# Performance work log

Measured on AMD Instinct MI355X. Metric: run time of the kernel, lower is better.

## Reference

```python
import jax, jax.numpy as jnp
import numpy as np

HIDDEN = 512
WINDOW = 5  # window_size default
NEG = -1000000000.0  # masked_fill value in the original


def setup_inputs() -> dict:
    key = jax.random.key(0)
    k0, k1, k2, k3, k4 = jax.random.split(key, 5)
    B, S, H = 32, 4096, HIDDEN
    decoder_hidden = jax.random.normal(k0, (B, H), dtype=jnp.float32)
    encoder_outputs = jax.random.normal(k1, (B, S, H), dtype=jnp.float32)
    input_lengths = jax.random.randint(k2, (B,), 1, S + 1)
    # position_network: nn.Linear(H, 1) -> weight [1,H], bias [1]
    Wp = jax.random.normal(k3, (1, H), dtype=jnp.float32) * (1.0 / np.sqrt(H))
    bp = jnp.zeros((1,), dtype=jnp.float32)
    # W_a: nn.Linear(H, H, bias=False) -> weight [H,H]
    Wa = jax.random.normal(k4, (H, H), dtype=jnp.float32) * (1.0 / np.sqrt(H))
    return {
        "decoder_hidden": decoder_hidden,
        "encoder_outputs": encoder_outputs,
        "Wp": Wp,
        "bp": bp,
        "Wa": Wa,
        "input_lengths": input_lengths,
    }


def reference(decoder_hidden, encoder_outputs, Wp, bp, Wa, input_lengths):
    B, S, H = encoder_outputs.shape
    half = WINDOW // 2

    # predicted window center: sigmoid(Linear(dh)) * S, truncated to int
    pos = jax.nn.sigmoid(decoder_hidden @ Wp.T + bp)[:, 0] * S  # [B]
    center = jnp.floor(pos).astype(jnp.int32)                   # int(...) on >=0 floats
    left = jnp.maximum(0, center - half)                        # [B]
    right = jnp.minimum(S, center + half + 1)                   # [B]

    idx = jnp.arange(S)                                         # [S]
    window_mask = (idx[None, :] >= left[:, None]) & (idx[None, :] < right[:, None])

    # 'general' score: dh_i @ (W_a enc_j) == (dh_i @ Wa) . enc_j
    q = decoder_hidden @ Wa                                     # [B,H]
    scores = jnp.einsum('bh,bsh->bs', q, encoder_outputs)       # [B,S]
    scores = jnp.where(window_mask, scores, 0.0)                # zeros outside window

    valid = idx[None, :] < input_lengths[:, None]               # length mask
    scores = jnp.where(valid, scores, NEG)

    attention_weights = jax.nn.softmax(scores, axis=1)          # [B,S]
    context_vector = jnp.einsum('bs,bsh->bh', attention_weights, encoder_outputs)
    return context_vector, attention_weights
```

## Files before the change

kernel.cpp:

```cpp
#include <hip/hip_runtime.h>

#define BB 32
#define SS 4096
#define HH 512
#define HALF 2


__global__ __launch_bounds__(256) void prep_kernel(
    const float* __restrict__ dh, const float* __restrict__ enc,
    const float* __restrict__ Wp, const float* __restrict__ bp,
    const float* __restrict__ Wa, const int* __restrict__ lens,
    float* __restrict__ wpar, int* __restrict__ ipar)
{
    int b = blockIdx.x;
    int tid = threadIdx.x;
    __shared__ float s_dh[HH];
    __shared__ float s_q[HH];
    __shared__ float red[256];
    __shared__ float s_scores[8];
    __shared__ int s_left, s_right, s_rend;

    for (int i = tid; i < HH; i += 256) s_dh[i] = dh[b * HH + i];
    __syncthreads();

    float p = 0.f;
    for (int i = tid; i < HH; i += 256) p += s_dh[i] * Wp[i];
    red[tid] = p;
    __syncthreads();
    for (int o = 128; o > 0; o >>= 1) {
        if (tid < o) red[tid] += red[tid + o];
        __syncthreads();
    }
    if (tid == 0) {
        float x = red[0] + bp[0];
        float sig = 1.f / (1.f + expf(-x));
        float pos = sig * (float)SS;
        int center = (int)floorf(pos);
        int left = center - HALF; if (left < 0) left = 0;
        int right = center + HALF + 1; if (right > SS) right = SS;
        int len = lens[b];
        s_left = left;
        s_right = right;
        s_rend = (right < len) ? right : len;
    }
    __syncthreads();

    for (int j = tid; j < HH; j += 256) {
        float acc = 0.f;
        #pragma unroll 8
        for (int i = 0; i < HH; ++i) acc += s_dh[i] * Wa[i * HH + j];
        s_q[j] = acc;
    }
    __syncthreads();

    int wave = tid >> 6, lane = tid & 63;
    const float* encb = enc + (size_t)b * SS * HH;
    for (int wi = wave; wi < 5; wi += 4) {
        int s = s_left + wi;
        float sc = 0.f;
        if (s < s_right) {
            const float* row = encb + (size_t)s * HH;
            for (int i = lane; i < HH; i += 64) sc += s_q[i] * row[i];
        }
        #pragma unroll
        for (int o = 32; o > 0; o >>= 1) sc += __shfl_down(sc, o);
        if (lane == 0) s_scores[wi] = sc;
    }
    __syncthreads();

    if (tid == 0) {
        int len = lens[b];
        int nwin = s_rend - s_left; if (nwin < 0) nwin = 0;
        int nonwin = len - nwin;
        float m = (nonwin > 0) ? 0.f : -3.0e38f;
        for (int i = 0; i < nwin; ++i) m = fmaxf(m, s_scores[i]);
        float e0 = expf(-m);
        float Z = (float)nonwin * e0;
        float wv[5];
        #pragma unroll
        for (int i = 0; i < 5; ++i) wv[i] = 0.f;
        for (int i = 0; i < nwin; ++i) { wv[i] = expf(s_scores[i] - m); Z += wv[i]; }
        float inv = 1.f / Z;
        wpar[b * 8 + 0] = e0 * inv;
        #pragma unroll
        for (int i = 0; i < 5; ++i) wpar[b * 8 + 1 + i] = wv[i] * inv;
        ipar[b * 4 + 0] = s_left;
        ipar[b * 4 + 1] = s_rend;
        ipar[b * 4 + 2] = len;
    }
}

__global__ __launch_bounds__(256) void weights_kernel(
    const float* __restrict__ wpar, const int* __restrict__ ipar,
    float* __restrict__ wout)
{
    int idx = blockIdx.x * 256 + threadIdx.x;
    int b = idx >> 12;
    int s = idx & (SS - 1);
    int left = ipar[b * 4 + 0];
    int rend = ipar[b * 4 + 1];
    int len  = ipar[b * 4 + 2];
    float w;
    if (s >= len) w = 0.f;
    else if (s >= left && s < rend) w = wpar[b * 8 + 1 + (s - left)];
    else w = wpar[b * 8];
    wout[idx] = w;
}

#define CS 64

__global__ __launch_bounds__(256) void context_kernel(
    const float* __restrict__ enc, const float* __restrict__ wpar,
    const int* __restrict__ ipar, float* __restrict__ ctx)
{
    const int nchunks = SS / CS;
    int b = blockIdx.x / nchunks;
    int chunk = blockIdx.x % nchunks;
    int len = ipar[b * 4 + 2];
    int s0 = chunk * CS;
    if (s0 >= len) return;
    int s1 = s0 + CS; if (s1 > len) s1 = len;
    int left = ipar[b * 4 + 0];
    int rend = ipar[b * 4 + 1];
    float c = wpar[b * 8];

    int tid = threadIdx.x;
    int col = tid & 127;
    int rp = tid >> 7;
    const float4* enc4 = (const float4*)(enc + (size_t)b * SS * HH);

    float4 acc = make_float4(0.f, 0.f, 0.f, 0.f);
    for (int s = s0 + rp; s < s1; s += 2) {
        float w = c;
        if (s >= left && s < rend) w = wpar[b * 8 + 1 + (s - left)];
        float4 v = enc4[(size_t)s * (HH / 4) + col];
        acc.x += w * v.x; acc.y += w * v.y; acc.z += w * v.z; acc.w += w * v.w;
    }

    __shared__ float4 part[128];
    if (rp == 1) part[col] = acc;
    __syncthreads();
    if (rp == 0) {
        float4 o = part[col];
        acc.x += o.x; acc.y += o.y; acc.z += o.z; acc.w += o.w;
        float* dst = ctx + b * HH + col * 4;
        atomicAdd(dst + 0, acc.x);
        atomicAdd(dst + 1, acc.y);
        atomicAdd(dst + 2, acc.z);
        atomicAdd(dst + 3, acc.w);
    }
}

extern "C" void kernel_launch(void* const* d_in, const int* in_sizes, int n_in,
                              void* d_out, int out_size, void* d_ws, size_t ws_size,
                              hipStream_t stream)
{
    const float* dh   = (const float*)d_in[0];
    const float* enc  = (const float*)d_in[1];
    const float* Wp   = (const float*)d_in[2];
    const float* bp   = (const float*)d_in[3];
    const float* Wa   = (const float*)d_in[4];
    const int*   lens = (const int*)d_in[5];

    float* ctx  = (float*)d_out;
    float* wout = (float*)d_out + BB * HH;

    float* wpar = (float*)d_ws;
    int*   ipar = (int*)((char*)d_ws + BB * 8 * sizeof(float));

    hipMemsetAsync(d_out, 0, BB * HH * sizeof(float), stream);

    prep_kernel<<<BB, 256, 0, stream>>>(dh, enc, Wp, bp, Wa, lens, wpar, ipar);
    weights_kernel<<<BB * SS / 256, 256, 0, stream>>>(wpar, ipar, wout);
    context_kernel<<<BB * (SS / CS), 256, 0, stream>>>(enc, wpar, ipar, ctx);
}
```

Before: 412.4 us.

## Fuse weights and context kernels, fold ctx zeroing into prep, widen prep block

New measurement: 376.5 us. 8.7% less time.

```diff
diff --git a/kernel.cpp b/kernel.cpp
--- a/kernel.cpp
+++ b/kernel.cpp
@@ -4,30 +4,31 @@
 #define SS 4096
 #define HH 512
 #define HALF 2
+#define CS 64
 
 
-__global__ __launch_bounds__(256) void prep_kernel(
+__global__ __launch_bounds__(512) void prep_kernel(
     const float* __restrict__ dh, const float* __restrict__ enc,
     const float* __restrict__ Wp, const float* __restrict__ bp,
     const float* __restrict__ Wa, const int* __restrict__ lens,
-    float* __restrict__ wpar, int* __restrict__ ipar)
+    float* __restrict__ wpar, int* __restrict__ ipar, float* __restrict__ ctx)
 {
     int b = blockIdx.x;
     int tid = threadIdx.x;
     __shared__ float s_dh[HH];
     __shared__ float s_q[HH];
-    __shared__ float red[256];
+    __shared__ float red[512];
     __shared__ float s_scores[8];
-    __shared__ int s_left, s_right, s_rend;
+    __shared__ int s_left, s_rend;
 
-    for (int i = tid; i < HH; i += 256) s_dh[i] = dh[b * HH + i];
+    ctx[b * HH + tid] = 0.f;
+
+    s_dh[tid] = dh[b * HH + tid];
     __syncthreads();
 
-    float p = 0.f;
-    for (int i = tid; i < HH; i += 256) p += s_dh[i] * Wp[i];
-    red[tid] = p;
+    red[tid] = s_dh[tid] * Wp[tid];
     __syncthreads();
-    for (int o = 128; o > 0; o >>= 1) {
+    for (int o = 256; o > 0; o >>= 1) {
         if (tid < o) red[tid] += red[tid + o];
         __syncthreads();
     }
@@ -40,31 +41,29 @@
         int right = center + HALF + 1; if (right > SS) right = SS;
         int len = lens[b];
         s_left = left;
-        s_right = right;
         s_rend = (right < len) ? right : len;
     }
     __syncthreads();
 
-    for (int j = tid; j < HH; j += 256) {
+    {
         float acc = 0.f;
         #pragma unroll 8
-        for (int i = 0; i < HH; ++i) acc += s_dh[i] * Wa[i * HH + j];
-        s_q[j] = acc;
+        for (int i = 0; i < HH; ++i) acc += s_dh[i] * Wa[i * HH + tid];
+        s_q[tid] = acc;
     }
     __syncthreads();
 
     int wave = tid >> 6, lane = tid & 63;
-    const float* encb = enc + (size_t)b * SS * HH;
-    for (int wi = wave; wi < 5; wi += 4) {
-        int s = s_left + wi;
+    if (wave < 5) {
+        int s = s_left + wave;
         float sc = 0.f;
-        if (s < s_right) {
-            const float* row = encb + (size_t)s * HH;
+        if (s < s_rend) {
+            const float* row = enc + (size_t)b * SS * HH + (size_t)s * HH;
             for (int i = lane; i < HH; i += 64) sc += s_q[i] * row[i];
         }
         #pragma unroll
         for (int o = 32; o > 0; o >>= 1) sc += __shfl_down(sc, o);
-        if (lane == 0) s_scores[wi] = sc;
+        if (lane == 0) s_scores[wave] = sc;
     }
     __syncthreads();
 
@@ -90,41 +89,32 @@
     }
 }
 
-__global__ __launch_bounds__(256) void weights_kernel(
-    const float* __restrict__ wpar, const int* __restrict__ ipar,
+__global__ __launch_bounds__(256) void ctxw_kernel(
+    const float* __restrict__ enc, const float* __restrict__ wpar,
+    const int* __restrict__ ipar, float* __restrict__ ctx,
     float* __restrict__ wout)
 {
-    int idx = blockIdx.x * 256 + threadIdx.x;
-    int b = idx >> 12;
-    int s = idx & (SS - 1);
+    int b = blockIdx.x >> 6;
+    int chunk = blockIdx.x & 63;
+    int s0 = chunk * CS;
     int left = ipar[b * 4 + 0];
     int rend = ipar[b * 4 + 1];
     int len  = ipar[b * 4 + 2];
-    float w;
-    if (s >= len) w = 0.f;
-    else if (s >= left && s < rend) w = wpar[b * 8 + 1 + (s - left)];
-    else w = wpar[b * 8];
-    wout[idx] = w;
-}
+    float c = wpar[b * 8];
+    int tid = threadIdx.x;
 
-#define CS 64
+    if (tid < CS) {
+        int s = s0 + tid;
+        float w;
+        if (s >= len) w = 0.f;
+        else if (s >= left && s < rend) w = wpar[b * 8 + 1 + (s - left)];
+        else w = c;
+        wout[b * SS + s] = w;
+    }
 
-__global__ __launch_bounds__(256) void context_kernel(
-    const float* __restrict__ enc, const float* __restrict__ wpar,
-    const int* __restrict__ ipar, float* __restrict__ ctx)
-{
-    const int nchunks = SS / CS;
-    int b = blockIdx.x / nchunks;
-    int chunk = blockIdx.x % nchunks;
-    int len = ipar[b * 4 + 2];
-    int s0 = chunk * CS;
     if (s0 >= len) return;
     int s1 = s0 + CS; if (s1 > len) s1 = len;
-    int left = ipar[b * 4 + 0];
-    int rend = ipar[b * 4 + 1];
-    float c = wpar[b * 8];
 
-    int tid = threadIdx.x;
     int col = tid & 127;
     int rp = tid >> 7;
     const float4* enc4 = (const float4*)(enc + (size_t)b * SS * HH);
@@ -168,9 +158,6 @@
     float* wpar = (float*)d_ws;
     int*   ipar = (int*)((char*)d_ws + BB * 8 * sizeof(float));
 
-    hipMemsetAsync(d_out, 0, BB * HH * sizeof(float), stream);
-
-    prep_kernel<<<BB, 256, 0, stream>>>(dh, enc, Wp, bp, Wa, lens, wpar, ipar);
-    weights_kernel<<<BB * SS / 256, 256, 0, stream>>>(wpar, ipar, wout);
-    context_kernel<<<BB * (SS / CS), 256, 0, stream>>>(enc, wpar, ipar, ctx);
+    prep_kernel<<<BB, 512, 0, stream>>>(dh, enc, Wp, bp, Wa, lens, wpar, ipar, ctx);
+    ctxw_kernel<<<BB * (SS / CS), 256, 0, stream>>>(enc, wpar, ipar, ctx, wout);
 }
```
